# Kernel optimization log

Hardware: AMD Instinct MI355X
Metric: run time of the kernel (lower is better)

Reference implementation:

```python
import jax, jax.numpy as jnp
import numpy as np

DIM = 256
HEADS = 8
K_RATIO = 0.25


def setup_inputs() -> dict:
    key = jax.random.key(0)
    ks = jax.random.split(key, 5)
    B, C, S = 4, DIM, 2048
    x = jax.random.normal(ks[0], (B, C, S), dtype=jnp.float32)
    # Conv1d(dim, 3*dim, 1, bias=False) weight -> (3*dim, dim)
    W_qkv = jax.random.normal(ks[1], (3 * DIM, DIM), dtype=jnp.float32) * (1.0 / np.sqrt(DIM))
    # depthwise Conv1d(3*dim, 3*dim, 3, groups=3*dim) weight -> (3*dim, 1, 3)
    W_dw = jax.random.normal(ks[2], (3 * DIM, 1, 3), dtype=jnp.float32) * (1.0 / np.sqrt(3))
    # Conv1d(dim, dim, 1, bias=False) weight -> (dim, dim)
    W_proj = jax.random.normal(ks[3], (DIM, DIM), dtype=jnp.float32) * (1.0 / np.sqrt(DIM))
    temperature = jnp.ones((HEADS, 1, 1), dtype=jnp.float32)
    return {"x": x, "W_qkv": W_qkv, "W_dw": W_dw, "W_proj": W_proj,
            "temperature": temperature}


def _l2norm(t, eps=1e-12):
    # F.normalize: x / max(||x||_2, eps)
    n = jnp.sqrt(jnp.sum(t * t, axis=-1, keepdims=True))
    return t / jnp.maximum(n, eps)


def reference(x, W_qkv, W_dw, W_proj, temperature):
    B, C, S = x.shape
    H = temperature.shape[0]
    hd = C // H
    # 1x1 conv == channel matmul
    qkv = jnp.einsum('oc,bcs->bos', W_qkv, x)  # [B, 3C, S]
    # depthwise conv, kernel 3, pad 1
    qkv = jax.lax.conv_general_dilated(
        qkv, W_dw, window_strides=(1,), padding=[(1, 1)],
        dimension_numbers=('NCH', 'OIH', 'NCH'),
        feature_group_count=3 * C)
    q, k, v = jnp.split(qkv, 3, axis=1)  # each [B, C, S]

    def to_heads(t):
        return t.reshape(B, H, hd, S).transpose(0, 1, 3, 2)  # [B, H, S, hd]

    q = _l2norm(to_heads(q))
    k = _l2norm(to_heads(k))
    v = to_heads(v)

    scores = jnp.einsum('bhsc,bhtc->bhst', q, k) * temperature  # [B,H,S,S]

    topk = max(1, min(S, int(np.ceil(K_RATIO * S))))
    vals, idx = jax.lax.top_k(scores, topk)  # [B,H,S,topk]

    # scatter top-k values into a -inf tensor along the last axis
    N = B * H * S
    sparse = jnp.full((N, S), -jnp.inf, dtype=scores.dtype)
    rows = jnp.arange(N)[:, None]
    sparse = sparse.at[rows, idx.reshape(N, topk)].set(vals.reshape(N, topk))
    sparse = jnp.clip(sparse.reshape(B, H, S, S), -10000.0, 10000.0)

    attn = jax.nn.softmax(sparse, axis=-1)  # dropout p=0.0 -> identity
    out = jnp.einsum('bhst,bhtc->bhsc', attn, v)  # [B,H,S,hd]
    out = out.transpose(0, 1, 3, 2).reshape(B, C, S)  # b (head c) s
    return jnp.einsum('oc,bcs->bos', W_proj, out)
```

## Files before the change

kernel.cpp:

```cpp
#include <hip/hip_runtime.h>
#include <math.h>

typedef __attribute__((ext_vector_type(8))) short short8;
typedef __attribute__((ext_vector_type(4))) float f32x4;

#define DEV __device__ __forceinline__

static constexpr int B_ = 4, C_ = 256, S_ = 2048, H_ = 8, O3_ = 768;
static constexpr int TOPK = 512;
static constexpr int QT = 16;
static constexpr int HCOLS = 1024;
static constexpr int HSTR = 1028;
static constexpr int PSTH = 1024;
static constexpr size_t K3_LDS_BYTES = (size_t)QT * HSTR * 4;

DEV unsigned short f2bf(float f) {
  unsigned u = __float_as_uint(f);
  return (unsigned short)((u + 0x7FFFu + ((u >> 16) & 1u)) >> 16);
}
DEV float bf2f(unsigned short h) { return __uint_as_float(((unsigned)h) << 16); }

__global__ void k_convw(const float* __restrict__ wqkv, const float* __restrict__ wproj,
                        unsigned short* __restrict__ wq_hi, unsigned short* __restrict__ wq_lo,
                        unsigned short* __restrict__ wproj_bf) {
  int i = blockIdx.x * 256 + threadIdx.x;
  if (i < O3_ * C_) {
    float f = wqkv[i];
    unsigned short h = f2bf(f);
    wq_hi[i] = h;
    wq_lo[i] = f2bf(f - bf2f(h));
  }
  if (i < C_ * C_) wproj_bf[i] = f2bf(wproj[i]);
}

__global__ void k_xt(const float* __restrict__ x, unsigned short* __restrict__ xT_hi,
                     unsigned short* __restrict__ xT_lo) {
  __shared__ float t[32][33];
  int b = blockIdx.z;
  int c0 = blockIdx.y * 32, s0 = blockIdx.x * 32;
  int tx = threadIdx.x, ty = threadIdx.y;
  const float* xb = x + (size_t)b * C_ * S_;
#pragma unroll
  for (int j = 0; j < 4; ++j)
    t[ty + 8 * j][tx] = xb[(size_t)(c0 + ty + 8 * j) * S_ + s0 + tx];
  __syncthreads();
  unsigned short* hb = xT_hi + (size_t)b * S_ * C_;
  unsigned short* lb = xT_lo + (size_t)b * S_ * C_;
#pragma unroll
  for (int j = 0; j < 4; ++j) {
    float f = t[tx][ty + 8 * j];
    unsigned short h = f2bf(f);
    size_t o = (size_t)(s0 + ty + 8 * j) * C_ + c0 + tx;
    hb[o] = h;
    lb[o] = f2bf(f - bf2f(h));
  }
}

__global__ __launch_bounds__(256) void k_qkv(const unsigned short* __restrict__ w_hi,
                                             const unsigned short* __restrict__ w_lo,
                                             const unsigned short* __restrict__ x_hi,
                                             const unsigned short* __restrict__ x_lo,
                                             float* __restrict__ raw) {
  int b = blockIdx.z;
  int m0 = blockIdx.y * 64, n0 = blockIdx.x * 64;
  int tid = threadIdx.x, lane = tid & 63, wid = tid >> 6;
  int l15 = lane & 15, lh = lane >> 4;
  int wm = (wid >> 1) * 32, wn = (wid & 1) * 32;
  const unsigned short* xhb = x_hi + (size_t)b * S_ * C_;
  const unsigned short* xlb = x_lo + (size_t)b * S_ * C_;
  f32x4 acc[2][2] = {};
  int mA = m0 + wm + l15;
  int nB = n0 + wn + l15;
  for (int k0 = 0; k0 < C_; k0 += 32) {
    int kk = k0 + lh * 8;
    short8 a0h = *(const short8*)(w_hi + (size_t)mA * C_ + kk);
    short8 a1h = *(const short8*)(w_hi + (size_t)(mA + 16) * C_ + kk);
    short8 a0l = *(const short8*)(w_lo + (size_t)mA * C_ + kk);
    short8 a1l = *(const short8*)(w_lo + (size_t)(mA + 16) * C_ + kk);
    short8 b0h = *(const short8*)(xhb + (size_t)nB * C_ + kk);
    short8 b1h = *(const short8*)(xhb + (size_t)(nB + 16) * C_ + kk);
    short8 b0l = *(const short8*)(xlb + (size_t)nB * C_ + kk);
    short8 b1l = *(const short8*)(xlb + (size_t)(nB + 16) * C_ + kk);
    acc[0][0] = __builtin_amdgcn_mfma_f32_16x16x32_bf16(a0h, b0h, acc[0][0], 0, 0, 0);
    acc[0][1] = __builtin_amdgcn_mfma_f32_16x16x32_bf16(a0h, b1h, acc[0][1], 0, 0, 0);
    acc[1][0] = __builtin_amdgcn_mfma_f32_16x16x32_bf16(a1h, b0h, acc[1][0], 0, 0, 0);
    acc[1][1] = __builtin_amdgcn_mfma_f32_16x16x32_bf16(a1h, b1h, acc[1][1], 0, 0, 0);
    acc[0][0] = __builtin_amdgcn_mfma_f32_16x16x32_bf16(a0h, b0l, acc[0][0], 0, 0, 0);
    acc[0][1] = __builtin_amdgcn_mfma_f32_16x16x32_bf16(a0h, b1l, acc[0][1], 0, 0, 0);
    acc[1][0] = __builtin_amdgcn_mfma_f32_16x16x32_bf16(a1h, b0l, acc[1][0], 0, 0, 0);
    acc[1][1] = __builtin_amdgcn_mfma_f32_16x16x32_bf16(a1h, b1l, acc[1][1], 0, 0, 0);
    acc[0][0] = __builtin_amdgcn_mfma_f32_16x16x32_bf16(a0l, b0h, acc[0][0], 0, 0, 0);
    acc[0][1] = __builtin_amdgcn_mfma_f32_16x16x32_bf16(a0l, b1h, acc[0][1], 0, 0, 0);
    acc[1][0] = __builtin_amdgcn_mfma_f32_16x16x32_bf16(a1l, b0h, acc[1][0], 0, 0, 0);
    acc[1][1] = __builtin_amdgcn_mfma_f32_16x16x32_bf16(a1l, b1h, acc[1][1], 0, 0, 0);
  }
  float* rawb = raw + (size_t)b * O3_ * S_;
#pragma unroll
  for (int i = 0; i < 2; ++i)
#pragma unroll
    for (int j = 0; j < 2; ++j)
#pragma unroll
      for (int r = 0; r < 4; ++r) {
        int row = m0 + wm + i * 16 + lh * 4 + r;
        int col = n0 + wn + j * 16 + l15;
        rawb[(size_t)row * S_ + col] = acc[i][j][r];
      }
}

DEV float conv3(const float* __restrict__ rp, const float* __restrict__ w, int s) {
  float a = (s > 0) ? rp[s - 1] : 0.f;
  float b = rp[s];
  float c = (s < S_ - 1) ? rp[s + 1] : 0.f;
  return w[0] * a + w[1] * b + w[2] * c;
}

__global__ __launch_bounds__(256) void k_dwnorm(const float* __restrict__ raw,
                                                const float* __restrict__ wdw,
                                                const float* __restrict__ temp,
                                                unsigned short* __restrict__ q_hi,
                                                unsigned short* __restrict__ q_lo,
                                                unsigned short* __restrict__ k_hi,
                                                unsigned short* __restrict__ k_lo,
                                                unsigned short* __restrict__ vt) {
  int b = blockIdx.z, h = blockIdx.y;
  int s = blockIdx.x * 256 + threadIdx.x;
  const float* rawb = raw + (size_t)b * O3_ * S_;
  float tph = temp[h];
  float qv[32], kv[32];
  float sq = 0.f, sk = 0.f;
  size_t bh = (size_t)(b * H_ + h);
#pragma unroll
  for (int d = 0; d < 32; ++d) {
    int oq = h * 32 + d;
    float q = conv3(rawb + (size_t)oq * S_, wdw + oq * 3, s);
    qv[d] = q; sq += q * q;
    int ok = oq + 256;
    float k = conv3(rawb + (size_t)ok * S_, wdw + ok * 3, s);
    kv[d] = k; sk += k * k;
    int ov = oq + 512;
    float v = conv3(rawb + (size_t)ov * S_, wdw + ov * 3, s);
    vt[(bh * 32 + d) * S_ + s] = f2bf(v);
  }
  float iq = tph / fmaxf(sqrtf(sq), 1e-12f);
  float ik = 1.f / fmaxf(sqrtf(sk), 1e-12f);
  size_t base = (bh * S_ + s) * 32;
#pragma unroll
  for (int d = 0; d < 32; ++d) {
    float qf = qv[d] * iq;
    unsigned short qh = f2bf(qf);
    q_hi[base + d] = qh;
    q_lo[base + d] = f2bf(qf - bf2f(qh));
    float kf = kv[d] * ik;
    unsigned short kh = f2bf(kf);
    k_hi[base + d] = kh;
    k_lo[base + d] = f2bf(kf - bf2f(kh));
  }
}

__global__ __launch_bounds__(1024, 8) void k_attn(const unsigned short* __restrict__ q_hi,
                                                  const unsigned short* __restrict__ q_lo,
                                                  const unsigned short* __restrict__ k_hi,
                                                  const unsigned short* __restrict__ k_lo,
                                                  const unsigned short* __restrict__ vt,
                                                  unsigned short* __restrict__ ao) {
  extern __shared__ float smem[];
  float* sc = smem;
  unsigned short* P = (unsigned short*)smem;
  float* red = smem;
  int bid = blockIdx.x;
  int tile = bid & 127;
  int bh = bid >> 7;
  int q0 = tile * QT;
  int tid = threadIdx.x, lane = tid & 63, wv = tid >> 6;
  int l15 = lane & 15, lh = lane >> 4;
  const unsigned short* vb = vt + (size_t)bh * 32 * S_;

  size_t qoff = ((size_t)bh * S_ + q0 + l15) * 32 + lh * 8;
  short8 ah = *(const short8*)(q_hi + qoff);
  short8 al = *(const short8*)(q_lo + qoff);
  size_t kbase = (size_t)bh * S_ * 32;

  float v[32];

#pragma unroll
  for (int hhalf = 0; hhalf < 2; ++hhalf) {
    int colbase = wv * 64;
    const unsigned short* khp = k_hi + kbase + (size_t)(hhalf * HCOLS + colbase + l15) * 32 + lh * 8;
    const unsigned short* klp = k_lo + kbase + (size_t)(hhalf * HCOLS + colbase + l15) * 32 + lh * 8;
    short8 kh0 = *(const short8*)(khp);
    short8 kl0 = *(const short8*)(klp);
    short8 kh1 = *(const short8*)(khp + 512);
    short8 kl1 = *(const short8*)(klp + 512);
    for (int nt = 0; nt < 4; ++nt) {
      short8 kh2 = kh1, kl2 = kl1;
      if (nt < 2) {
        kh2 = *(const short8*)(khp + (nt + 2) * 512);
        kl2 = *(const short8*)(klp + (nt + 2) * 512);
      }
      f32x4 d = {};
      d = __builtin_amdgcn_mfma_f32_16x16x32_bf16(ah, kh0, d, 0, 0, 0);
      d = __builtin_amdgcn_mfma_f32_16x16x32_bf16(ah, kl0, d, 0, 0, 0);
      d = __builtin_amdgcn_mfma_f32_16x16x32_bf16(al, kh0, d, 0, 0, 0);
      int tloc = colbase + nt * 16;
#pragma unroll
      for (int r = 0; r < 4; ++r)
        sc[(lh * 4 + r) * HSTR + tloc + l15] = d[r];
      kh0 = kh1; kl0 = kl1; kh1 = kh2; kl1 = kl2;
    }
    __syncthreads();
#pragma unroll
    for (int j = 0; j < 16; ++j)
      v[hhalf * 16 + j] = sc[wv * HSTR + lane + 64 * j];
    __syncthreads();
  }

  float vmax, ssum_is;
  {
    vmax = v[0];
    float vmin = v[0], sum = 0.f, sqs = 0.f;
#pragma unroll
    for (int j = 0; j < 32; ++j) {
      vmax = fmaxf(vmax, v[j]); vmin = fminf(vmin, v[j]);
      sum += v[j]; sqs = fmaf(v[j], v[j], sqs);
    }
#pragma unroll
    for (int m = 1; m < 64; m <<= 1) {
      vmax = fmaxf(vmax, __shfl_xor(vmax, m));
      vmin = fminf(vmin, __shfl_xor(vmin, m));
      sum += __shfl_xor(sum, m);
      sqs += __shfl_xor(sqs, m);
    }
    float mu = sum * (1.f / 2048.f);
    float sig = sqrtf(fmaxf(sqs * (1.f / 2048.f) - mu * mu, 0.f));

    float vlo = vmin - 1e-3f, vhi = vmax;
    float flo = 1536.f, fhi = -512.f;
    int chi = 0;
    float T = vhi;
    bool exact = false;
    int lastside = 0;
    float piv = mu + 0.67449f * sig;
    if (!(piv > vlo && piv < vhi)) piv = 0.5f * (vlo + vhi);
    for (int it = 0; it < 32; ++it) {
      int c = 0;
#pragma unroll
      for (int j = 0; j < 32; ++j)
        c += (int)__popcll(__ballot(v[j] > piv));
      if (c == TOPK) { T = piv; exact = true; break; }
      if (c > TOPK) {
        if (lastside == 1) fhi *= 0.5f;
        vlo = piv; flo = (float)(c - TOPK); lastside = 1;
      } else {
        if (lastside == -1) flo *= 0.5f;
        vhi = piv; fhi = (float)(c - TOPK); chi = c; lastside = -1;
      }
      piv = vhi - fhi * (vhi - vlo) / (fhi - flo);
      if (!(piv > vlo && piv < vhi)) piv = 0.5f * (vlo + vhi);
      if (!(piv > vlo && piv < vhi)) break;
    }
    int cntGT = exact ? TOPK : chi;
    if (!exact) T = vhi;

    unsigned selbits = 0;
#pragma unroll
    for (int j = 0; j < 32; ++j)
      if (v[j] > T) selbits |= (1u << j);
    int need = TOPK - cntGT;
    if (need > 0) {
      int base = 0;
      unsigned long long lmask = (lane == 0) ? 0ull : (~0ull >> (64 - lane));
#pragma unroll
      for (int j = 0; j < 32; ++j) {
        bool tie = (v[j] == T);
        unsigned long long m = __ballot(tie);
        int rank = base + (int)__popcll(m & lmask);
        if (tie && rank < need) selbits |= (1u << j);
        base += (int)__popcll(m);
      }
    }

    float ssum = 0.f;
#pragma unroll
    for (int j = 0; j < 32; ++j) {
      float e = ((selbits >> j) & 1u) ? __expf(v[j] - vmax) : 0.f;
      v[j] = e;
      ssum += e;
    }
#pragma unroll
    for (int m = 1; m < 64; m <<= 1) ssum += __shfl_xor(ssum, m);
    ssum_is = 1.f / ssum;
  }

  f32x4 acc0 = {}, acc1 = {};
  int swz_w = (wv & 7) << 3;
  int swz_r = (l15 & 7) << 3;
#pragma unroll
  for (int hhalf = 0; hhalf < 2; ++hhalf) {
#pragma unroll
    for (int j = 0; j < 16; ++j) {
      int jj = hhalf * 16 + j;
      int idx = (wv * PSTH + j * 64 + lane) ^ swz_w;
      P[idx] = f2bf(v[jj] * ssum_is);
    }
    __syncthreads();
    {
      const unsigned short* v0p = vb + (size_t)l15 * S_ + hhalf * HCOLS + wv * 64 + lh * 8;
      const unsigned short* v1p = v0p + 16 * S_;
#pragma unroll
      for (int kt = 0; kt < 2; ++kt) {
        int lc = wv * 64 + kt * 32 + lh * 8;
        int pidx = (l15 * PSTH + lc) ^ swz_r;
        short8 a = *(const short8*)(P + pidx);
        short8 b0 = *(const short8*)(v0p + kt * 32);
        short8 b1 = *(const short8*)(v1p + kt * 32);
        acc0 = __builtin_amdgcn_mfma_f32_16x16x32_bf16(a, b0, acc0, 0, 0, 0);
        acc1 = __builtin_amdgcn_mfma_f32_16x16x32_bf16(a, b1, acc1, 0, 0, 0);
      }
    }
    __syncthreads();
  }

#pragma unroll
  for (int r = 0; r < 4; ++r) {
    red[wv * 529 + (lh * 4 + r) * 33 + l15] = acc0[r];
    red[wv * 529 + (lh * 4 + r) * 33 + 16 + l15] = acc1[r];
  }
  __syncthreads();
  if (tid < 512) {
    int row = tid >> 5, d = tid & 31;
    float s = 0.f;
#pragma unroll
    for (int w = 0; w < 16; ++w) s += red[w * 529 + row * 33 + d];
    ao[((size_t)bh * S_ + q0 + row) * 32 + d] = f2bf(s);
  }
}

__global__ __launch_bounds__(256) void k_proj(const unsigned short* __restrict__ wbf,
                                              const unsigned short* __restrict__ ao,
                                              float* __restrict__ out) {
  int b = blockIdx.z;
  int m0 = blockIdx.y * 64, n0 = blockIdx.x * 64;
  int tid = threadIdx.x, lane = tid & 63, wid = tid >> 6;
  int l15 = lane & 15, lh = lane >> 4;
  int wm = (wid >> 1) * 32, wn = (wid & 1) * 32;
  const unsigned short* aob = ao + (size_t)b * H_ * S_ * 32;
  f32x4 acc[2][2] = {};
  int mA = m0 + wm + l15;
  int nB = n0 + wn + l15;
  for (int k0 = 0; k0 < C_; k0 += 32) {
    int kk = k0 + lh * 8;
    int hh = kk >> 5;
    int dd = kk & 31;
    short8 a0 = *(const short8*)(wbf + (size_t)mA * C_ + kk);
    short8 a1 = *(const short8*)(wbf + (size_t)(mA + 16) * C_ + kk);
    short8 b0 = *(const short8*)(aob + ((size_t)hh * S_ + nB) * 32 + dd);
    short8 b1 = *(const short8*)(aob + ((size_t)hh * S_ + nB + 16) * 32 + dd);
    acc[0][0] = __builtin_amdgcn_mfma_f32_16x16x32_bf16(a0, b0, acc[0][0], 0, 0, 0);
    acc[0][1] = __builtin_amdgcn_mfma_f32_16x16x32_bf16(a0, b1, acc[0][1], 0, 0, 0);
    acc[1][0] = __builtin_amdgcn_mfma_f32_16x16x32_bf16(a1, b0, acc[1][0], 0, 0, 0);
    acc[1][1] = __builtin_amdgcn_mfma_f32_16x16x32_bf16(a1, b1, acc[1][1], 0, 0, 0);
  }
  float* ob = out + (size_t)b * C_ * S_;
#pragma unroll
  for (int i = 0; i < 2; ++i)
#pragma unroll
    for (int j = 0; j < 2; ++j)
#pragma unroll
      for (int r = 0; r < 4; ++r) {
        int row = m0 + wm + i * 16 + lh * 4 + r;
        int col = n0 + wn + j * 16 + l15;
        ob[(size_t)row * S_ + col] = acc[i][j][r];
      }
}

extern "C" void kernel_launch(void* const* d_in, const int* in_sizes, int n_in,
                              void* d_out, int out_size, void* d_ws, size_t ws_size,
                              hipStream_t stream) {
  const float* x = (const float*)d_in[0];
  const float* wqkv = (const float*)d_in[1];
  const float* wdw = (const float*)d_in[2];
  const float* wproj = (const float*)d_in[3];
  const float* temp = (const float*)d_in[4];
  float* out = (float*)d_out;

  char* ws = (char*)d_ws;
  size_t off = 0;
  auto alloc = [&](size_t bytes) -> void* {
    void* p = ws + off;
    off += (bytes + 255) & ~(size_t)255;
    return p;
  };
  unsigned short* x_hi     = (unsigned short*)alloc((size_t)B_ * S_ * C_ * 2);
  unsigned short* x_lo     = (unsigned short*)alloc((size_t)B_ * S_ * C_ * 2);
  unsigned short* wq_hi    = (unsigned short*)alloc((size_t)O3_ * C_ * 2);
  unsigned short* wq_lo    = (unsigned short*)alloc((size_t)O3_ * C_ * 2);
  unsigned short* wproj_bf = (unsigned short*)alloc((size_t)C_ * C_ * 2);
  float*          raw      = (float*)alloc((size_t)B_ * O3_ * S_ * 4);
  unsigned short* k_hi     = (unsigned short*)alloc((size_t)B_ * H_ * S_ * 32 * 2);
  unsigned short* k_lo     = (unsigned short*)alloc((size_t)B_ * H_ * S_ * 32 * 2);
  unsigned short* vt       = (unsigned short*)alloc((size_t)B_ * H_ * 32 * S_ * 2);
  unsigned short* q_hi     = x_hi;
  unsigned short* q_lo     = x_lo;
  unsigned short* ao       = (unsigned short*)raw;

  (void)hipFuncSetAttribute(reinterpret_cast<const void*>(k_attn),
                            hipFuncAttributeMaxDynamicSharedMemorySize, (int)K3_LDS_BYTES);

  k_convw<<<dim3((O3_ * C_ + 255) / 256), dim3(256), 0, stream>>>(wqkv, wproj, wq_hi, wq_lo, wproj_bf);
  k_xt<<<dim3(S_ / 32, C_ / 32, B_), dim3(32, 8), 0, stream>>>(x, x_hi, x_lo);
  k_qkv<<<dim3(S_ / 64, O3_ / 64, B_), dim3(256), 0, stream>>>(wq_hi, wq_lo, x_hi, x_lo, raw);
  k_dwnorm<<<dim3(S_ / 256, H_, B_), dim3(256), 0, stream>>>(raw, wdw, temp, q_hi, q_lo, k_hi, k_lo, vt);
  k_attn<<<dim3(B_ * H_ * (S_ / QT)), dim3(1024), K3_LDS_BYTES, stream>>>(q_hi, q_lo, k_hi, k_lo, vt, ao);
  k_proj<<<dim3(S_ / 64, C_ / 64, B_), dim3(256), 0, stream>>>(wproj_bf, ao, out);
}
```

Measured before the change: 293.3 us.

## Use hardware bf16 packing, reshape dwnorm threads, speed top-k pivot search

Replaces the software round-to-bf16 with the packed v_cvt_pk_bf16_f32 instruction and adds a hi/lo split helper. The depthwise-conv/normalize kernel is reorganized so 8 lanes share one position, with shuffle-reduced norms and vectorized packed stores, launching more blocks. In attention, the first secant step of the threshold search uses a Gaussian-density Newton estimate to cut iterations. Softmax normalization is moved to after the P·V reduction, and V loads are hoisted before the barrier. Deferring normalization changes bf16 rounding of P slightly.

```diff
diff --git a/kernel.cpp b/kernel.cpp
--- a/kernel.cpp
+++ b/kernel.cpp
@@ -3,6 +3,7 @@
 
 typedef __attribute__((ext_vector_type(8))) short short8;
 typedef __attribute__((ext_vector_type(4))) float f32x4;
+typedef __attribute__((ext_vector_type(2))) unsigned int uint2v;
 
 #define DEV __device__ __forceinline__
 
@@ -14,23 +15,31 @@
 static constexpr int PSTH = 1024;
 static constexpr size_t K3_LDS_BYTES = (size_t)QT * HSTR * 4;
 
-DEV unsigned short f2bf(float f) {
-  unsigned u = __float_as_uint(f);
-  return (unsigned short)((u + 0x7FFFu + ((u >> 16) & 1u)) >> 16);
-}
+DEV unsigned cvt_pk_bf16(float a, float b) {
+  unsigned r;
+  asm("v_cvt_pk_bf16_f32 %0, %1, %2" : "=v"(r) : "v"(a), "v"(b));
+  return r;
+}
+DEV unsigned short f2bf1(float f) { return (unsigned short)(cvt_pk_bf16(f, f) & 0xFFFFu); }
 DEV float bf2f(unsigned short h) { return __uint_as_float(((unsigned)h) << 16); }
+DEV void hilo(float f, unsigned short& h, unsigned short& l) {
+  unsigned p = cvt_pk_bf16(f, f);
+  h = (unsigned short)p;
+  float r = f - __uint_as_float(p << 16);
+  l = (unsigned short)(cvt_pk_bf16(r, r) & 0xFFFFu);
+}
 
 __global__ void k_convw(const float* __restrict__ wqkv, const float* __restrict__ wproj,
                         unsigned short* __restrict__ wq_hi, unsigned short* __restrict__ wq_lo,
                         unsigned short* __restrict__ wproj_bf) {
   int i = blockIdx.x * 256 + threadIdx.x;
   if (i < O3_ * C_) {
-    float f = wqkv[i];
-    unsigned short h = f2bf(f);
+    unsigned short h, l;
+    hilo(wqkv[i], h, l);
     wq_hi[i] = h;
-    wq_lo[i] = f2bf(f - bf2f(h));
-  }
-  if (i < C_ * C_) wproj_bf[i] = f2bf(wproj[i]);
+    wq_lo[i] = l;
+  }
+  if (i < C_ * C_) wproj_bf[i] = f2bf1(wproj[i]);
 }
 
 __global__ void k_xt(const float* __restrict__ x, unsigned short* __restrict__ xT_hi,
@@ -48,11 +57,11 @@
   unsigned short* lb = xT_lo + (size_t)b * S_ * C_;
 #pragma unroll
   for (int j = 0; j < 4; ++j) {
-    float f = t[tx][ty + 8 * j];
-    unsigned short h = f2bf(f);
+    unsigned short h, l;
+    hilo(t[tx][ty + 8 * j], h, l);
     size_t o = (size_t)(s0 + ty + 8 * j) * C_ + c0 + tx;
     hb[o] = h;
-    lb[o] = f2bf(f - bf2f(h));
+    lb[o] = l;
   }
 }
 
@@ -123,37 +132,59 @@
                                                 unsigned short* __restrict__ k_lo,
                                                 unsigned short* __restrict__ vt) {
   int b = blockIdx.z, h = blockIdx.y;
-  int s = blockIdx.x * 256 + threadIdx.x;
+  int tid = threadIdx.x;
+  int wave = tid >> 6, lane = tid & 63;
+  int dg = lane & 7;
+  int sl = lane >> 3;
+  int s = blockIdx.x * 32 + wave * 8 + sl;
   const float* rawb = raw + (size_t)b * O3_ * S_;
   float tph = temp[h];
-  float qv[32], kv[32];
+  size_t bh = (size_t)(b * H_ + h);
+  float qv[4], kv[4], vv[4];
   float sq = 0.f, sk = 0.f;
-  size_t bh = (size_t)(b * H_ + h);
-#pragma unroll
-  for (int d = 0; d < 32; ++d) {
+#pragma unroll
+  for (int dd = 0; dd < 4; ++dd) {
+    int d = dg * 4 + dd;
     int oq = h * 32 + d;
     float q = conv3(rawb + (size_t)oq * S_, wdw + oq * 3, s);
-    qv[d] = q; sq += q * q;
+    qv[dd] = q; sq += q * q;
     int ok = oq + 256;
     float k = conv3(rawb + (size_t)ok * S_, wdw + ok * 3, s);
-    kv[d] = k; sk += k * k;
+    kv[dd] = k; sk += k * k;
     int ov = oq + 512;
-    float v = conv3(rawb + (size_t)ov * S_, wdw + ov * 3, s);
-    vt[(bh * 32 + d) * S_ + s] = f2bf(v);
+    vv[dd] = conv3(rawb + (size_t)ov * S_, wdw + ov * 3, s);
+  }
+#pragma unroll
+  for (int m = 1; m < 8; m <<= 1) {
+    sq += __shfl_xor(sq, m);
+    sk += __shfl_xor(sk, m);
   }
   float iq = tph / fmaxf(sqrtf(sq), 1e-12f);
   float ik = 1.f / fmaxf(sqrtf(sk), 1e-12f);
-  size_t base = (bh * S_ + s) * 32;
-#pragma unroll
-  for (int d = 0; d < 32; ++d) {
-    float qf = qv[d] * iq;
-    unsigned short qh = f2bf(qf);
-    q_hi[base + d] = qh;
-    q_lo[base + d] = f2bf(qf - bf2f(qh));
-    float kf = kv[d] * ik;
-    unsigned short kh = f2bf(kf);
-    k_hi[base + d] = kh;
-    k_lo[base + d] = f2bf(kf - bf2f(kh));
+  size_t base = (bh * S_ + s) * 32 + dg * 4;
+
+  float q0 = qv[0] * iq, q1 = qv[1] * iq, q2 = qv[2] * iq, q3 = qv[3] * iq;
+  unsigned qh01 = cvt_pk_bf16(q0, q1), qh23 = cvt_pk_bf16(q2, q3);
+  *(uint2v*)(q_hi + base) = uint2v{qh01, qh23};
+  float ql0 = q0 - __uint_as_float(qh01 << 16);
+  float ql1 = q1 - __uint_as_float(qh01 & 0xFFFF0000u);
+  float ql2 = q2 - __uint_as_float(qh23 << 16);
+  float ql3 = q3 - __uint_as_float(qh23 & 0xFFFF0000u);
+  *(uint2v*)(q_lo + base) = uint2v{cvt_pk_bf16(ql0, ql1), cvt_pk_bf16(ql2, ql3)};
+
+  float k0 = kv[0] * ik, k1 = kv[1] * ik, k2 = kv[2] * ik, k3 = kv[3] * ik;
+  unsigned kh01 = cvt_pk_bf16(k0, k1), kh23 = cvt_pk_bf16(k2, k3);
+  *(uint2v*)(k_hi + base) = uint2v{kh01, kh23};
+  float kl0 = k0 - __uint_as_float(kh01 << 16);
+  float kl1 = k1 - __uint_as_float(kh01 & 0xFFFF0000u);
+  float kl2 = k2 - __uint_as_float(kh23 << 16);
+  float kl3 = k3 - __uint_as_float(kh23 & 0xFFFF0000u);
+  *(uint2v*)(k_lo + base) = uint2v{cvt_pk_bf16(kl0, kl1), cvt_pk_bf16(kl2, kl3)};
+
+#pragma unroll
+  for (int dd = 0; dd < 4; ++dd) {
+    int d = dg * 4 + dd;
+    vt[(bh * 32 + d) * S_ + s] = f2bf1(vv[dd]);
   }
 }
 
@@ -164,6 +195,7 @@
                                                   const unsigned short* __restrict__ vt,
                                                   unsigned short* __restrict__ ao) {
   extern __shared__ float smem[];
+  __shared__ float is_arr[QT];
   float* sc = smem;
   unsigned short* P = (unsigned short*)smem;
   float* red = smem;
@@ -214,7 +246,7 @@
     __syncthreads();
   }
 
-  float vmax, ssum_is;
+  float vmax;
   {
     vmax = v[0];
     float vmin = v[0], sum = 0.f, sqs = 0.f;
@@ -254,9 +286,17 @@
         if (lastside == -1) flo *= 0.5f;
         vhi = piv; fhi = (float)(c - TOPK); chi = c; lastside = -1;
       }
-      piv = vhi - fhi * (vhi - vlo) / (fhi - flo);
-      if (!(piv > vlo && piv < vhi)) piv = 0.5f * (vlo + vhi);
-      if (!(piv > vlo && piv < vhi)) break;
+      float npiv;
+      if (it == 0 && sig > 1e-20f) {
+        float z = (piv - mu) / sig;
+        float dens = 0.398942f * __expf(-0.5f * z * z) * (2048.f / sig);
+        npiv = piv + (float)(c - TOPK) / fmaxf(dens, 1e-6f);
+      } else {
+        npiv = vhi - fhi * (vhi - vlo) / (fhi - flo);
+      }
+      if (!(npiv > vlo && npiv < vhi)) npiv = 0.5f * (vlo + vhi);
+      if (!(npiv > vlo && npiv < vhi)) break;
+      piv = npiv;
     }
     int cntGT = exact ? TOPK : chi;
     if (!exact) T = vhi;
@@ -288,7 +328,7 @@
     }
 #pragma unroll
     for (int m = 1; m < 64; m <<= 1) ssum += __shfl_xor(ssum, m);
-    ssum_is = 1.f / ssum;
+    if (lane == 0) is_arr[wv] = 1.f / ssum;
   }
 
   f32x4 acc0 = {}, acc1 = {};
@@ -296,26 +336,26 @@
   int swz_r = (l15 & 7) << 3;
 #pragma unroll
   for (int hhalf = 0; hhalf < 2; ++hhalf) {
+    const unsigned short* v0p = vb + (size_t)l15 * S_ + hhalf * HCOLS + wv * 64 + lh * 8;
+    const unsigned short* v1p = v0p + 16 * S_;
+    short8 b00 = *(const short8*)(v0p);
+    short8 b10 = *(const short8*)(v1p);
+    short8 b01 = *(const short8*)(v0p + 32);
+    short8 b11 = *(const short8*)(v1p + 32);
 #pragma unroll
     for (int j = 0; j < 16; ++j) {
-      int jj = hhalf * 16 + j;
       int idx = (wv * PSTH + j * 64 + lane) ^ swz_w;
-      P[idx] = f2bf(v[jj] * ssum_is);
+      P[idx] = f2bf1(v[hhalf * 16 + j]);
     }
     __syncthreads();
     {
-      const unsigned short* v0p = vb + (size_t)l15 * S_ + hhalf * HCOLS + wv * 64 + lh * 8;
-      const unsigned short* v1p = v0p + 16 * S_;
-#pragma unroll
-      for (int kt = 0; kt < 2; ++kt) {
-        int lc = wv * 64 + kt * 32 + lh * 8;
-        int pidx = (l15 * PSTH + lc) ^ swz_r;
-        short8 a = *(const short8*)(P + pidx);
-        short8 b0 = *(const short8*)(v0p + kt * 32);
-        short8 b1 = *(const short8*)(v1p + kt * 32);
-        acc0 = __builtin_amdgcn_mfma_f32_16x16x32_bf16(a, b0, acc0, 0, 0, 0);
-        acc1 = __builtin_amdgcn_mfma_f32_16x16x32_bf16(a, b1, acc1, 0, 0, 0);
-      }
+      int lc0 = wv * 64 + lh * 8;
+      short8 a0 = *(const short8*)(P + ((l15 * PSTH + lc0) ^ swz_r));
+      short8 a1 = *(const short8*)(P + ((l15 * PSTH + lc0 + 32) ^ swz_r));
+      acc0 = __builtin_amdgcn_mfma_f32_16x16x32_bf16(a0, b00, acc0, 0, 0, 0);
+      acc1 = __builtin_amdgcn_mfma_f32_16x16x32_bf16(a0, b10, acc1, 0, 0, 0);
+      acc0 = __builtin_amdgcn_mfma_f32_16x16x32_bf16(a1, b01, acc0, 0, 0, 0);
+      acc1 = __builtin_amdgcn_mfma_f32_16x16x32_bf16(a1, b11, acc1, 0, 0, 0);
     }
     __syncthreads();
   }
@@ -331,7 +371,8 @@
     float s = 0.f;
 #pragma unroll
     for (int w = 0; w < 16; ++w) s += red[w * 529 + row * 33 + d];
-    ao[((size_t)bh * S_ + q0 + row) * 32 + d] = f2bf(s);
+    s *= is_arr[row];
+    ao[((size_t)bh * S_ + q0 + row) * 32 + d] = f2bf1(s);
   }
 }
 
@@ -409,7 +450,7 @@
   k_convw<<<dim3((O3_ * C_ + 255) / 256), dim3(256), 0, stream>>>(wqkv, wproj, wq_hi, wq_lo, wproj_bf);
   k_xt<<<dim3(S_ / 32, C_ / 32, B_), dim3(32, 8), 0, stream>>>(x, x_hi, x_lo);
   k_qkv<<<dim3(S_ / 64, O3_ / 64, B_), dim3(256), 0, stream>>>(wq_hi, wq_lo, x_hi, x_lo, raw);
-  k_dwnorm<<<dim3(S_ / 256, H_, B_), dim3(256), 0, stream>>>(raw, wdw, temp, q_hi, q_lo, k_hi, k_lo, vt);
+  k_dwnorm<<<dim3(S_ / 32, H_, B_), dim3(256), 0, stream>>>(raw, wdw, temp, q_hi, q_lo, k_hi, k_lo, vt);
   k_attn<<<dim3(B_ * H_ * (S_ / QT)), dim3(1024), K3_LDS_BYTES, stream>>>(q_hi, q_lo, k_hi, k_lo, vt, ao);
   k_proj<<<dim3(S_ / 64, C_ / 64, B_), dim3(256), 0, stream>>>(wproj_bf, ao, out);
 }
```

Result: no change. 290.8 us (-0.9%).
